# Performance work log

Measured on AMD Instinct MI355X. Metric: run time of the kernel, lower is better.

## Reference

```python
import jax, jax.numpy as jnp
import numpy as np

N_NODES = 100000
N_EDGES = 1600000
IN_FEATS = 128
H1 = 256
H2 = 256
N_CLASSES = 64


def setup_inputs() -> dict:
    key = jax.random.key(0)
    ks = jax.random.split(key, 12)
    x = jax.random.normal(ks[0], (N_NODES, IN_FEATS), dtype=jnp.float32)
    src = jax.random.randint(ks[1], (N_EDGES,), 0, N_NODES, dtype=jnp.int64 if jax.config.jax_enable_x64 else jnp.int32)
    dst = jax.random.randint(ks[2], (N_EDGES,), 0, N_NODES, dtype=jnp.int64 if jax.config.jax_enable_x64 else jnp.int32)
    def lin(kw, kb, fan_in, fan_out):
        bound = 1.0 / np.sqrt(fan_in)
        W = jax.random.uniform(kw, (fan_out, fan_in), minval=-bound, maxval=bound, dtype=jnp.float32)
        b = jax.random.uniform(kb, (fan_out,), minval=-bound, maxval=bound, dtype=jnp.float32)
        return W, b
    W1, b1 = lin(ks[3], ks[4], 2 * IN_FEATS, H1)
    W2, b2 = lin(ks[5], ks[6], 2 * H1, H2)
    W3, b3 = lin(ks[7], ks[8], 2 * H2, N_CLASSES)
    return {"x": x, "src": src, "dst": dst,
            "W1": W1, "b1": b1, "W2": W2, "b2": b2, "W3": W3, "b3": b3}


def _sage_conv(h, src, dst, W, b):
    # message = copy from src node, reduce = mean at dst node (DGL copy_u + mean)
    m = jnp.take(h, src, axis=0)                                  # [E, d]
    s = jax.ops.segment_sum(m, dst, num_segments=N_NODES)         # [N, d]
    deg = jax.ops.segment_sum(jnp.ones((m.shape[0],), h.dtype), dst,
                              num_segments=N_NODES)               # [N]
    h_N = s / jnp.maximum(deg, 1.0)[:, None]                      # isolated nodes -> 0 (DGL behavior)
    h_total = jnp.concatenate([h, h_N], axis=1)                   # [N, 2d]
    return h_total @ W.T + b                                      # dropout inactive at eval (p=0.05)


def reference(x, src, dst, W1, b1, W2, b2, W3, b3):
    h = jax.nn.relu(_sage_conv(x, src, dst, W1, b1))
    h = jax.nn.relu(_sage_conv(h, src, dst, W2, b2))
    return _sage_conv(h, src, dst, W3, b3)
```

## Files before the change

### kernel.cpp

```cpp
#include <hip/hip_runtime.h>
#include <hip/hip_bf16.h>
#include <cstdint>
#include <cstddef>

#define N_NODES 100000
#define N_EDGES 1600000
#define NBUCK   128
#define NPB     782
#define NB_E    ((N_EDGES + 4095) / 4096)

typedef __attribute__((ext_vector_type(8))) short short8;
typedef __attribute__((ext_vector_type(4))) float floatx4;

__device__ inline float bf_lo(unsigned int u) { return __uint_as_float(u << 16); }
__device__ inline float bf_hi(unsigned int u) { return __uint_as_float(u & 0xffff0000u); }
__device__ inline unsigned short f2bf(float f) {
  unsigned int u = __float_as_uint(f);
  u += 0x7fffu + ((u >> 16) & 1u);
  return (unsigned short)(u >> 16);
}

__global__ void cvt_f32_bf16(const float* __restrict__ in,
                             unsigned short* __restrict__ out, int n4) {
  int t = blockIdx.x * blockDim.x + threadIdx.x;
  if (t >= n4) return;
  float4 v = ((const float4*)in)[t];
  ushort4 o;
  o.x = f2bf(v.x); o.y = f2bf(v.y); o.z = f2bf(v.z); o.w = f2bf(v.w);
  ((ushort4*)out)[t] = o;
}

__global__ void cvt_w3cat(const float* __restrict__ W3, unsigned short* __restrict__ out) {
  int t = blockIdx.x * blockDim.x + threadIdx.x;
  if (t >= 128 * 256 / 4) return;
  int idx4 = t * 4;
  int r = idx4 >> 8, c = idx4 & 255;
  float4 v = *(const float4*)(W3 + (size_t)(r & 63) * 512 + (r >> 6) * 256 + c);
  ushort4 o;
  o.x = f2bf(v.x); o.y = f2bf(v.y); o.z = f2bf(v.z); o.w = f2bf(v.w);
  *(ushort4*)(out + (size_t)r * 256 + c) = o;
}

__device__ inline int wave_incl_scan(int v, int lane) {
#pragma unroll
  for (int off = 1; off < 64; off <<= 1) {
    int t = __shfl_up(v, off, 64);
    if (lane >= off) v += t;
  }
  return v;
}

__global__ __launch_bounds__(256)
void pass1a_kernel(const int* __restrict__ dst, int* __restrict__ bucketCount) {
  __shared__ int hist[NBUCK];
  if (threadIdx.x < NBUCK) hist[threadIdx.x] = 0;
  __syncthreads();
#pragma unroll
  for (int i = 0; i < 16; ++i) {
    int e = blockIdx.x * 4096 + i * 256 + threadIdx.x;
    if (e < N_EDGES) atomicAdd(&hist[dst[e] / NPB], 1);
  }
  __syncthreads();
  if (threadIdx.x < NBUCK) atomicAdd(&bucketCount[threadIdx.x], hist[threadIdx.x]);
}

__global__ void scanB_kernel(const int* __restrict__ bucketCount,
                             int* __restrict__ bucketBase, int* __restrict__ gCursorB) {
  __shared__ int wsum[2];
  int t = threadIdx.x, lane = t & 63, wid = t >> 6;
  int v = bucketCount[t];
  int incl = wave_incl_scan(v, lane);
  if (lane == 63) wsum[wid] = incl;
  __syncthreads();
  int off = (wid == 1) ? wsum[0] : 0;
  bucketBase[t] = off + incl - v;
  gCursorB[t]   = off + incl - v;
  if (t == 127) bucketBase[NBUCK] = off + incl;
}

__global__ __launch_bounds__(256)
void pass1b_kernel(const int* __restrict__ src, const int* __restrict__ dst,
                   int* __restrict__ gCursorB, unsigned int* __restrict__ staging) {
  __shared__ int hist[NBUCK];
  if (threadIdx.x < NBUCK) hist[threadIdx.x] = 0;
  __syncthreads();
#pragma unroll
  for (int i = 0; i < 16; ++i) {
    int e = blockIdx.x * 4096 + i * 256 + threadIdx.x;
    if (e < N_EDGES) atomicAdd(&hist[dst[e] / NPB], 1);
  }
  __syncthreads();
  if (threadIdx.x < NBUCK)
    hist[threadIdx.x] = atomicAdd(&gCursorB[threadIdx.x], hist[threadIdx.x]);
  __syncthreads();
#pragma unroll
  for (int i = 0; i < 16; ++i) {
    int e = blockIdx.x * 4096 + i * 256 + threadIdx.x;
    if (e < N_EDGES) {
      int d = dst[e];
      int b = d / NPB;
      int pos = atomicAdd(&hist[b], 1);
      staging[pos] = (unsigned)src[e] | ((unsigned)(d - b * NPB) << 17);
    }
  }
}

__global__ __launch_bounds__(1024)
void pass2_kernel(const unsigned int* __restrict__ staging, const int* __restrict__ bucketBase,
                  int* __restrict__ start, float* __restrict__ invdeg,
                  int* __restrict__ esrc) {
  __shared__ int cnt[1024];
  __shared__ int cur[1024];
  __shared__ int wsum[16];
  const int b = blockIdx.x, tid = threadIdx.x;
  const int lane = tid & 63, wid = tid >> 6;
  const int n0 = b * NPB, n1 = min(n0 + NPB, N_NODES);
  const int nLocal = n1 - n0;
  const int p0 = bucketBase[b], p1 = bucketBase[b + 1];

  cnt[tid] = 0;
  __syncthreads();
  for (int e = p0 + tid; e < p1; e += 1024)
    atomicAdd(&cnt[staging[e] >> 17], 1);
  __syncthreads();

  int c = cnt[tid];
  int incl = wave_incl_scan(c, lane);
  if (lane == 63) wsum[wid] = incl;
  __syncthreads();
  if (wid == 0) {
    int v = (lane < 16) ? wsum[lane] : 0;
    int i2 = wave_incl_scan(v, lane);
    if (lane < 16) wsum[lane] = i2 - v;
  }
  __syncthreads();
  int excl = wsum[wid] + incl - c;
  cur[tid] = excl;
  if (tid < nLocal) {
    start[n0 + tid] = p0 + excl;
    invdeg[n0 + tid] = 1.0f / fmaxf((float)c, 1.0f);
  }
  if (b == NBUCK - 1 && tid == 0) start[N_NODES] = N_EDGES;
  __syncthreads();

  for (int e = p0 + tid; e < p1; e += 1024) {
    unsigned int pr = staging[e];
    int pos = p0 + atomicAdd(&cur[pr >> 17], 1);
    esrc[pos] = (int)(pr & 0x1FFFFu);
  }
}

template<int D>
__global__ __launch_bounds__(256)
void gather_mean(const unsigned short* __restrict__ h,
                 const int* __restrict__ start,
                 const int* __restrict__ esrc,
                 const float* __restrict__ invdeg,
                 unsigned short* __restrict__ hn) {
  int wave = (int)((blockIdx.x * 256 + threadIdx.x) >> 6);
  if (wave >= N_NODES) return;
  int lane = threadIdx.x & 63;
  int s0 = start[wave], s1 = start[wave + 1];
  constexpr int FPL = D / 64;
  float acc[FPL] = {};
  const unsigned short* base = h + lane * FPL;

  int e = s0;
  if constexpr (FPL == 4) {
    for (; e + 4 <= s1; e += 4) {
      int sn0 = esrc[e], sn1 = esrc[e + 1], sn2 = esrc[e + 2], sn3 = esrc[e + 3];
      uint2 p0 = *(const uint2*)(base + (size_t)sn0 * D);
      uint2 p1 = *(const uint2*)(base + (size_t)sn1 * D);
      uint2 p2 = *(const uint2*)(base + (size_t)sn2 * D);
      uint2 p3 = *(const uint2*)(base + (size_t)sn3 * D);
      acc[0] += bf_lo(p0.x) + bf_lo(p1.x) + bf_lo(p2.x) + bf_lo(p3.x);
      acc[1] += bf_hi(p0.x) + bf_hi(p1.x) + bf_hi(p2.x) + bf_hi(p3.x);
      acc[2] += bf_lo(p0.y) + bf_lo(p1.y) + bf_lo(p2.y) + bf_lo(p3.y);
      acc[3] += bf_hi(p0.y) + bf_hi(p1.y) + bf_hi(p2.y) + bf_hi(p3.y);
    }
    for (; e < s1; ++e) {
      int sn = esrc[e];
      uint2 p = *(const uint2*)(base + (size_t)sn * D);
      acc[0] += bf_lo(p.x); acc[1] += bf_hi(p.x);
      acc[2] += bf_lo(p.y); acc[3] += bf_hi(p.y);
    }
  } else {
    for (; e + 4 <= s1; e += 4) {
      int sn0 = esrc[e], sn1 = esrc[e + 1], sn2 = esrc[e + 2], sn3 = esrc[e + 3];
      unsigned int p0 = *(const unsigned int*)(base + (size_t)sn0 * D);
      unsigned int p1 = *(const unsigned int*)(base + (size_t)sn1 * D);
      unsigned int p2 = *(const unsigned int*)(base + (size_t)sn2 * D);
      unsigned int p3 = *(const unsigned int*)(base + (size_t)sn3 * D);
      acc[0] += bf_lo(p0) + bf_lo(p1) + bf_lo(p2) + bf_lo(p3);
      acc[1] += bf_hi(p0) + bf_hi(p1) + bf_hi(p2) + bf_hi(p3);
    }
    for (; e < s1; ++e) {
      int sn = esrc[e];
      unsigned int p = *(const unsigned int*)(base + (size_t)sn * D);
      acc[0] += bf_lo(p); acc[1] += bf_hi(p);
    }
  }

  float inv = invdeg[wave];
  unsigned short* out = hn + (size_t)wave * D + lane * FPL;
  if constexpr (FPL == 4) {
    ushort4 o;
    o.x = f2bf(acc[0] * inv); o.y = f2bf(acc[1] * inv);
    o.z = f2bf(acc[2] * inv); o.w = f2bf(acc[3] * inv);
    *(ushort4*)out = o;
  } else {
    ushort2 o;
    o.x = f2bf(acc[0] * inv); o.y = f2bf(acc[1] * inv);
    *(ushort2*)out = o;
  }
}

__global__ __launch_bounds__(256)
void gather_add64(const unsigned short* __restrict__ Y3,
                  const int* __restrict__ start, const int* __restrict__ esrc,
                  const float* __restrict__ invdeg, float* __restrict__ out) {
  int wave = (int)((blockIdx.x * 256 + threadIdx.x) >> 6);
  if (wave >= N_NODES) return;
  int lane = threadIdx.x & 63;
  int half = lane >> 5, l32 = lane & 31;
  int s0 = start[wave], s1 = start[wave + 1];
  float a0 = 0.f, a1 = 0.f;
  for (int e = s0 + half; e < s1; e += 2) {
    int sn = esrc[e];
    unsigned int p = *(const unsigned int*)(Y3 + (size_t)sn * 64 + 2 * l32);
    a0 += bf_lo(p); a1 += bf_hi(p);
  }
  a0 += __shfl_xor(a0, 32, 64);
  a1 += __shfl_xor(a1, 32, 64);
  if (half == 0) {
    float inv = invdeg[wave];
    float2* q = (float2*)(out + (size_t)wave * 64 + 2 * l32);
    float2 v = *q;
    v.x += inv * a0; v.y += inv * a1;
    *q = v;
  }
}

template<int D, int DOUT, int BN, bool RELU, bool OUTF32, int MODE>
__global__ __launch_bounds__(256)
void sage_gemm(const unsigned short* __restrict__ H,
               const unsigned short* __restrict__ HN,
               const unsigned short* __restrict__ Wb,
               const float* __restrict__ bias,
               void* __restrict__ outp,
               unsigned short* __restrict__ y3) {
  constexpr int K   = (MODE == 1) ? D : 2 * D;
  constexpr int BM  = 128, KC = 32;
  constexpr int NCHUNK = K / KC;
  constexpr int AF  = BM / 16;
  constexpr int BF  = BN / 16;
  constexpr int FR  = AF + BF;
  constexpr int NMF = 4;
  constexpr int NJF = BF / 2;

  __shared__ __align__(16) unsigned short lds0[FR * 512];
  __shared__ __align__(16) unsigned short lds1[FR * 512];

  const int tid  = threadIdx.x;
  const int wave = tid >> 6, lane = tid & 63;
  const int l16  = lane & 15, quad = lane >> 4;
  const int n0   = blockIdx.x * BM;
  const int bn0  = blockIdx.y * BN;
  const int wm   = wave >> 1, wn = wave & 1;

  floatx4 acc[NMF][NJF] = {};

  auto stage = [&](int c, unsigned short* buf) {
    const int kc = c * KC;
    const unsigned short* srcH = (kc < D) ? H : HN;
    const int kb = (kc < D) ? kc : kc - D;
    const int w0 = __builtin_amdgcn_readfirstlane(wave);
#pragma unroll
    for (int i = 0; i < FR / 4; ++i) {
      const int fu = w0 + 4 * i;
      const unsigned short* g;
      if (fu < AF) {
        int row = min(n0 + fu * 16 + l16, N_NODES - 1);
        g = srcH + (size_t)row * D + kb + quad * 8;
      } else {
        int col = bn0 + (fu - AF) * 16 + l16;
        g = Wb + (size_t)col * K + kc + quad * 8;
      }
      __builtin_amdgcn_global_load_lds(
          (const __attribute__((address_space(1))) unsigned int*)g,
          (__attribute__((address_space(3))) unsigned int*)(buf + fu * 512),
          16, 0, 0);
    }
  };

  auto compute = [&](const unsigned short* buf) {
    short8 b[NJF];
#pragma unroll
    for (int jt = 0; jt < NJF; ++jt)
      b[jt] = *(const short8*)(buf + (AF + wn * NJF + jt) * 512 + lane * 8);
#pragma unroll
    for (int mi = 0; mi < NMF; ++mi) {
      short8 a = *(const short8*)(buf + (wm * NMF + mi) * 512 + lane * 8);
#pragma unroll
      for (int jt = 0; jt < NJF; ++jt)
        acc[mi][jt] = __builtin_amdgcn_mfma_f32_16x16x32_bf16(a, b[jt], acc[mi][jt], 0, 0, 0);
    }
  };

  stage(0, lds0);
  __syncthreads();
#pragma unroll 1
  for (int c = 0; c < NCHUNK; c += 2) {
    stage(c + 1, lds1);
    compute(lds0);
    __syncthreads();
    if (c + 2 < NCHUNK) stage(c + 2, lds0);
    compute(lds1);
    __syncthreads();
  }

#pragma unroll
  for (int mi = 0; mi < NMF; ++mi) {
#pragma unroll
    for (int jt = 0; jt < NJF; ++jt) {
      int j = bn0 + wn * (NJF * 16) + jt * 16 + l16;
      float bj = (MODE == 1 && wn == 1) ? 0.0f : bias[j];
#pragma unroll
      for (int r = 0; r < 4; ++r) {
        int node = n0 + wm * 64 + mi * 16 + quad * 4 + r;
        if (node < N_NODES) {
          float v = acc[mi][jt][r];
          if constexpr (MODE == 1) {
            if (wn == 0) ((float*)outp)[(size_t)node * 64 + j] = v + bj;
            else y3[(size_t)node * 64 + (j - 64)] = f2bf(v);
          } else {
            v += bj;
            if (RELU) v = fmaxf(v, 0.0f);
            if (OUTF32) ((float*)outp)[(size_t)node * DOUT + j] = v;
            else ((unsigned short*)outp)[(size_t)node * DOUT + j] = f2bf(v);
          }
        }
      }
    }
  }
}

extern "C" void kernel_launch(void* const* d_in, const int* in_sizes, int n_in,
                              void* d_out, int out_size, void* d_ws, size_t ws_size,
                              hipStream_t stream) {
  const float* x   = (const float*)d_in[0];
  const int*   src = (const int*)d_in[1];
  const int*   dst = (const int*)d_in[2];
  const float* W1 = (const float*)d_in[3];
  const float* b1 = (const float*)d_in[4];
  const float* W2 = (const float*)d_in[5];
  const float* b2 = (const float*)d_in[6];
  const float* W3 = (const float*)d_in[7];
  const float* b3 = (const float*)d_in[8];

  char* ws = (char*)d_ws;
  unsigned short* H0 = (unsigned short*)ws; ws += (size_t)N_NODES * 128 * 2;
  unsigned short* H1 = (unsigned short*)ws; ws += (size_t)N_NODES * 256 * 2;
  unsigned short* H2 = (unsigned short*)ws; ws += (size_t)N_NODES * 256 * 2;
  unsigned short* HN = (unsigned short*)ws; ws += (size_t)N_NODES * 256 * 2;
  unsigned int* staging = (unsigned int*)ws; ws += (size_t)N_EDGES * 4;
  int* esrc   = (int*)ws;  ws += (size_t)N_EDGES * 4;
  int* startp = (int*)ws;  ws += (size_t)(N_NODES + 32) * 4;
  float* invdeg = (float*)ws; ws += (size_t)(N_NODES + 32) * 4;
  int* bucketCount = (int*)ws; ws += 512;
  int* bucketBase  = (int*)ws; ws += 1024;
  int* gCursorB    = (int*)ws; ws += 512;
  unsigned short* Y3 = (unsigned short*)ws; ws += (size_t)N_NODES * 64 * 2;
  unsigned short* Wb1 = (unsigned short*)ws; ws += 256 * 256 * 2;
  unsigned short* Wb2 = (unsigned short*)ws; ws += 256 * 512 * 2;
  unsigned short* Wb3 = (unsigned short*)ws; ws += 128 * 256 * 2;

  hipMemsetAsync(bucketCount, 0, NBUCK * 4, stream);
  pass1a_kernel<<<NB_E, 256, 0, stream>>>(dst, bucketCount);
  scanB_kernel<<<1, 128, 0, stream>>>(bucketCount, bucketBase, gCursorB);
  pass1b_kernel<<<NB_E, 256, 0, stream>>>(src, dst, gCursorB, staging);
  pass2_kernel<<<NBUCK, 1024, 0, stream>>>(staging, bucketBase, startp, invdeg, esrc);

  cvt_f32_bf16<<<(N_NODES * 128 / 4 + 255) / 256, 256, 0, stream>>>(x, H0, N_NODES * 128 / 4);
  cvt_f32_bf16<<<(256 * 256 / 4 + 255) / 256, 256, 0, stream>>>(W1, Wb1, 256 * 256 / 4);
  cvt_f32_bf16<<<(256 * 512 / 4 + 255) / 256, 256, 0, stream>>>(W2, Wb2, 256 * 512 / 4);
  cvt_w3cat<<<(128 * 256 / 4 + 255) / 256, 256, 0, stream>>>(W3, Wb3);

  const int GGRID = (N_NODES * 64 + 255) / 256;
  const int MG = (N_NODES + 127) / 128;

  gather_mean<128><<<GGRID, 256, 0, stream>>>(H0, startp, esrc, invdeg, HN);
  sage_gemm<128, 256, 128, true, false, 0><<<dim3(MG, 2), 256, 0, stream>>>(H0, HN, Wb1, b1, H1, nullptr);

  gather_mean<256><<<GGRID, 256, 0, stream>>>(H1, startp, esrc, invdeg, HN);
  sage_gemm<256, 256, 128, true, false, 0><<<dim3(MG, 2), 256, 0, stream>>>(H1, HN, Wb2, b2, H2, nullptr);

  sage_gemm<256, 128, 128, false, true, 1><<<dim3(MG, 1), 256, 0, stream>>>(H2, nullptr, Wb3, b3, (float*)d_out, Y3);
  gather_add64<<<GGRID, 256, 0, stream>>>(Y3, startp, esrc, invdeg, (float*)d_out);
}
```

Measured before the change: 614.9 us.

## Overlap neighbor gather with GEMM via chunked fused layer kernels

Replaces the separate gather_mean and sage_gemm launches for layers 1 and 2 with a fused kernel that, in each launch, runs GEMM tiles for one node chunk while gathering neighbor means for the next chunk. Nodes are split into four chunks, which gives a software pipeline across five launches per layer. The goal is to hide the memory-bound gather behind the compute-bound GEMM and make better use of the GPU. In exchange it adds launches, mixes LDS-heavy GEMM blocks with lightweight gather blocks (which may hurt occupancy), and uses a hand-written GEMM body whose tiling may differ from the original sage_gemm.

```diff
diff --git a/kernel.cpp b/kernel.cpp
--- a/kernel.cpp
+++ b/kernel.cpp
@@ -151,16 +151,18 @@
 }
 
 template<int D>
-__global__ __launch_bounds__(256)
-void gather_mean(const unsigned short* __restrict__ h,
+__device__ __forceinline__
+void gather_body(int gblk, int node0, int node1,
+                 const unsigned short* __restrict__ h,
                  const int* __restrict__ start,
                  const int* __restrict__ esrc,
                  const float* __restrict__ invdeg,
                  unsigned short* __restrict__ hn) {
-  int wave = (int)((blockIdx.x * 256 + threadIdx.x) >> 6);
-  if (wave >= N_NODES) return;
+  int w = (gblk * 256 + (int)threadIdx.x) >> 6;
+  int node = node0 + w;
+  if (node >= node1) return;
   int lane = threadIdx.x & 63;
-  int s0 = start[wave], s1 = start[wave + 1];
+  int s0 = start[node], s1 = start[node + 1];
   constexpr int FPL = D / 64;
   float acc[FPL] = {};
   const unsigned short* base = h + lane * FPL;
@@ -201,8 +203,8 @@
     }
   }
 
-  float inv = invdeg[wave];
-  unsigned short* out = hn + (size_t)wave * D + lane * FPL;
+  float inv = invdeg[node];
+  unsigned short* out = hn + (size_t)node * D + lane * FPL;
   if constexpr (FPL == 4) {
     ushort4 o;
     o.x = f2bf(acc[0] * inv); o.y = f2bf(acc[1] * inv);
@@ -212,6 +214,119 @@
     ushort2 o;
     o.x = f2bf(acc[0] * inv); o.y = f2bf(acc[1] * inv);
     *(ushort2*)out = o;
+  }
+}
+
+template<int D, bool RELU>
+__device__ __forceinline__
+void gemm_body(int bx, int by,
+               const unsigned short* __restrict__ H,
+               const unsigned short* __restrict__ HN,
+               const unsigned short* __restrict__ Wb,
+               const float* __restrict__ bias,
+               unsigned short* __restrict__ out) {
+  constexpr int K   = 2 * D;
+  constexpr int BM  = 128, KC = 32;
+  constexpr int NCHUNK = K / KC;
+  constexpr int AF  = 8, BF = 8, FR = 16;
+  constexpr int NMF = 4, NJF = 4;
+
+  __shared__ __align__(16) unsigned short lds0[FR * 512];
+  __shared__ __align__(16) unsigned short lds1[FR * 512];
+
+  const int tid  = threadIdx.x;
+  const int wave = tid >> 6, lane = tid & 63;
+  const int l16  = lane & 15, quad = lane >> 4;
+  const int n0   = bx * BM;
+  const int bn0  = by * 128;
+  const int wm   = wave >> 1, wn = wave & 1;
+
+  floatx4 acc[NMF][NJF] = {};
+
+  auto stage = [&](int c, unsigned short* buf) {
+    const int kc = c * KC;
+    const unsigned short* srcH = (kc < D) ? H : HN;
+    const int kb = (kc < D) ? kc : kc - D;
+    const int w0 = __builtin_amdgcn_readfirstlane(wave);
+#pragma unroll
+    for (int i = 0; i < FR / 4; ++i) {
+      const int fu = w0 + 4 * i;
+      const unsigned short* g;
+      if (fu < AF) {
+        int row = min(n0 + fu * 16 + l16, N_NODES - 1);
+        g = srcH + (size_t)row * D + kb + quad * 8;
+      } else {
+        int col = bn0 + (fu - AF) * 16 + l16;
+        g = Wb + (size_t)col * K + kc + quad * 8;
+      }
+      __builtin_amdgcn_global_load_lds(
+          (const __attribute__((address_space(1))) unsigned int*)g,
+          (__attribute__((address_space(3))) unsigned int*)(buf + fu * 512),
+          16, 0, 0);
+    }
+  };
+
+  auto compute = [&](const unsigned short* buf) {
+    short8 b[NJF];
+#pragma unroll
+    for (int jt = 0; jt < NJF; ++jt)
+      b[jt] = *(const short8*)(buf + (AF + wn * NJF + jt) * 512 + lane * 8);
+#pragma unroll
+    for (int mi = 0; mi < NMF; ++mi) {
+      short8 a = *(const short8*)(buf + (wm * NMF + mi) * 512 + lane * 8);
+#pragma unroll
+      for (int jt = 0; jt < NJF; ++jt)
+        acc[mi][jt] = __builtin_amdgcn_mfma_f32_16x16x32_bf16(a, b[jt], acc[mi][jt], 0, 0, 0);
+    }
+  };
+
+  stage(0, lds0);
+  __syncthreads();
+#pragma unroll 1
+  for (int c = 0; c < NCHUNK; c += 2) {
+    stage(c + 1, lds1);
+    compute(lds0);
+    __syncthreads();
+    if (c + 2 < NCHUNK) stage(c + 2, lds0);
+    compute(lds1);
+    __syncthreads();
+  }
+
+#pragma unroll
+  for (int mi = 0; mi < NMF; ++mi) {
+#pragma unroll
+    for (int jt = 0; jt < NJF; ++jt) {
+      int j = bn0 + wn * (NJF * 16) + jt * 16 + l16;
+      float bj = bias[j];
+#pragma unroll
+      for (int r = 0; r < 4; ++r) {
+        int node = n0 + wm * 64 + mi * 16 + quad * 4 + r;
+        if (node < N_NODES) {
+          float v = acc[mi][jt][r] + bj;
+          if (RELU) v = fmaxf(v, 0.0f);
+          out[(size_t)node * 256 + j] = f2bf(v);
+        }
+      }
+    }
+  }
+}
+
+template<int D, bool RELU>
+__global__ __launch_bounds__(256)
+void fused_layer(int tile0, int nGemmBlk, int node0, int node1,
+                 const unsigned short* __restrict__ H,
+                 unsigned short* __restrict__ HN,
+                 const unsigned short* __restrict__ Wb,
+                 const float* __restrict__ bias,
+                 unsigned short* __restrict__ Hout,
+                 const int* __restrict__ start,
+                 const int* __restrict__ esrc,
+                 const float* __restrict__ invdeg) {
+  int b = blockIdx.x;
+  if (b < nGemmBlk) {
+    gemm_body<D, RELU>(tile0 + (b >> 1), b & 1, H, HN, Wb, bias, Hout);
+  } else {
+    gather_body<D>(b - nGemmBlk, node0, node1, H, start, esrc, invdeg, HN);
   }
 }
 
@@ -386,15 +501,39 @@
   cvt_f32_bf16<<<(256 * 512 / 4 + 255) / 256, 256, 0, stream>>>(W2, Wb2, 256 * 512 / 4);
   cvt_w3cat<<<(128 * 256 / 4 + 255) / 256, 256, 0, stream>>>(W3, Wb3);
 
+  static const int tileC[5] = {0, 196, 392, 588, 782};
+  static const int nodeC[5] = {0, 25088, 50176, 75264, N_NODES};
+
+  {
+    int gb0 = (nodeC[1] - nodeC[0] + 3) / 4;
+    fused_layer<128, true><<<gb0, 256, 0, stream>>>(
+        0, 0, nodeC[0], nodeC[1], H0, HN, Wb1, b1, H1, startp, esrc, invdeg);
+    for (int c = 0; c < 4; ++c) {
+      int nG = (tileC[c + 1] - tileC[c]) * 2;
+      int n0g = (c < 3) ? nodeC[c + 1] : 0;
+      int n1g = (c < 3) ? nodeC[c + 2] : 0;
+      int ng  = (c < 3) ? (n1g - n0g + 3) / 4 : 0;
+      fused_layer<128, true><<<nG + ng, 256, 0, stream>>>(
+          tileC[c], nG, n0g, n1g, H0, HN, Wb1, b1, H1, startp, esrc, invdeg);
+    }
+  }
+
+  {
+    int gb0 = (nodeC[1] - nodeC[0] + 3) / 4;
+    fused_layer<256, true><<<gb0, 256, 0, stream>>>(
+        0, 0, nodeC[0], nodeC[1], H1, HN, Wb2, b2, H2, startp, esrc, invdeg);
+    for (int c = 0; c < 4; ++c) {
+      int nG = (tileC[c + 1] - tileC[c]) * 2;
+      int n0g = (c < 3) ? nodeC[c + 1] : 0;
+      int n1g = (c < 3) ? nodeC[c + 2] : 0;
+      int ng  = (c < 3) ? (n1g - n0g + 3) / 4 : 0;
+      fused_layer<256, true><<<nG + ng, 256, 0, stream>>>(
+          tileC[c], nG, n0g, n1g, H1, HN, Wb2, b2, H2, startp, esrc, invdeg);
+    }
+  }
+
+  const int MG = (N_NODES + 127) / 128;
   const int GGRID = (N_NODES * 64 + 255) / 256;
-  const int MG = (N_NODES + 127) / 128;
-
-  gather_mean<128><<<GGRID, 256, 0, stream>>>(H0, startp, esrc, invdeg, HN);
-  sage_gemm<128, 256, 128, true, false, 0><<<dim3(MG, 2), 256, 0, stream>>>(H0, HN, Wb1, b1, H1, nullptr);
-
-  gather_mean<256><<<GGRID, 256, 0, stream>>>(H1, startp, esrc, invdeg, HN);
-  sage_gemm<256, 256, 128, true, false, 0><<<dim3(MG, 2), 256, 0, stream>>>(H1, HN, Wb2, b2, H2, nullptr);
-
   sage_gemm<256, 128, 128, false, true, 1><<<dim3(MG, 1), 256, 0, stream>>>(H2, nullptr, Wb3, b3, (float*)d_out, Y3);
   gather_add64<<<GGRID, 256, 0, stream>>>(Y3, startp, esrc, invdeg, (float*)d_out);
 }
```

Result: slower. 778.5 us (+26.6%).

## Fuse preprocessing launches and use per-block histograms; unroll final gather loads

Applied to the files above, without the earlier changes.

Merges the dst histogram pass and all four fp32-to-bf16 conversions into a single front kernel. Each edge block now writes its own bucket histogram, so the scan kernel can compute per-block offsets. That removes the memset, the global atomics and the duplicate histogram pass in pass1b. It also makes the bucket scatter order deterministic. Separately, the final 64-wide gather now issues 8 independent loads per iteration into two accumulator pairs to raise memory-level parallelism. The cost is a serial loop over about 391 blocks in the single-block scan kernel.

```diff
diff --git a/kernel.cpp b/kernel.cpp
--- a/kernel.cpp
+++ b/kernel.cpp
@@ -8,6 +8,12 @@
 #define NBUCK   128
 #define NPB     782
 #define NB_E    ((N_EDGES + 4095) / 4096)
+
+#define FK_X    NB_E
+#define FK_W1   (FK_X + 12500)
+#define FK_W2   (FK_W1 + 64)
+#define FK_W3   (FK_W2 + 128)
+#define FK_END  (FK_W3 + 32)
 
 typedef __attribute__((ext_vector_type(8))) short short8;
 typedef __attribute__((ext_vector_type(4))) float floatx4;
@@ -20,25 +26,47 @@
   return (unsigned short)(u >> 16);
 }
 
-__global__ void cvt_f32_bf16(const float* __restrict__ in,
-                             unsigned short* __restrict__ out, int n4) {
-  int t = blockIdx.x * blockDim.x + threadIdx.x;
-  if (t >= n4) return;
+__device__ inline void cvt4_body(const float* __restrict__ in,
+                                 unsigned short* __restrict__ out, int t) {
   float4 v = ((const float4*)in)[t];
   ushort4 o;
   o.x = f2bf(v.x); o.y = f2bf(v.y); o.z = f2bf(v.z); o.w = f2bf(v.w);
   ((ushort4*)out)[t] = o;
 }
 
-__global__ void cvt_w3cat(const float* __restrict__ W3, unsigned short* __restrict__ out) {
-  int t = blockIdx.x * blockDim.x + threadIdx.x;
-  if (t >= 128 * 256 / 4) return;
-  int idx4 = t * 4;
-  int r = idx4 >> 8, c = idx4 & 255;
-  float4 v = *(const float4*)(W3 + (size_t)(r & 63) * 512 + (r >> 6) * 256 + c);
-  ushort4 o;
-  o.x = f2bf(v.x); o.y = f2bf(v.y); o.z = f2bf(v.z); o.w = f2bf(v.w);
-  *(ushort4*)(out + (size_t)r * 256 + c) = o;
+__global__ __launch_bounds__(256)
+void front_kernel(const int* __restrict__ dst, int* __restrict__ blockHist,
+                  const float* __restrict__ x,  unsigned short* __restrict__ H0,
+                  const float* __restrict__ W1, unsigned short* __restrict__ Wb1,
+                  const float* __restrict__ W2, unsigned short* __restrict__ Wb2,
+                  const float* __restrict__ W3, unsigned short* __restrict__ Wb3) {
+  __shared__ int hist[NBUCK];
+  const int b = blockIdx.x, tid = threadIdx.x;
+  if (b < FK_X) {
+    if (tid < NBUCK) hist[tid] = 0;
+    __syncthreads();
+#pragma unroll
+    for (int i = 0; i < 16; ++i) {
+      int e = b * 4096 + i * 256 + tid;
+      if (e < N_EDGES) atomicAdd(&hist[dst[e] / NPB], 1);
+    }
+    __syncthreads();
+    if (tid < NBUCK) blockHist[b * NBUCK + tid] = hist[tid];
+  } else if (b < FK_W1) {
+    cvt4_body(x, H0, (b - FK_X) * 256 + tid);
+  } else if (b < FK_W2) {
+    cvt4_body(W1, Wb1, (b - FK_W1) * 256 + tid);
+  } else if (b < FK_W3) {
+    cvt4_body(W2, Wb2, (b - FK_W2) * 256 + tid);
+  } else {
+    int t = (b - FK_W3) * 256 + tid;
+    int idx4 = t * 4;
+    int r = idx4 >> 8, c = idx4 & 255;
+    float4 v = *(const float4*)(W3 + (size_t)(r & 63) * 512 + (r >> 6) * 256 + c);
+    ushort4 o;
+    o.x = f2bf(v.x); o.y = f2bf(v.y); o.z = f2bf(v.z); o.w = f2bf(v.w);
+    *(ushort4*)(Wb3 + (size_t)r * 256 + c) = o;
+  }
 }
 
 __device__ inline int wave_incl_scan(int v, int lane) {
@@ -50,48 +78,33 @@
   return v;
 }
 
-__global__ __launch_bounds__(256)
-void pass1a_kernel(const int* __restrict__ dst, int* __restrict__ bucketCount) {
-  __shared__ int hist[NBUCK];
-  if (threadIdx.x < NBUCK) hist[threadIdx.x] = 0;
-  __syncthreads();
-#pragma unroll
-  for (int i = 0; i < 16; ++i) {
-    int e = blockIdx.x * 4096 + i * 256 + threadIdx.x;
-    if (e < N_EDGES) atomicAdd(&hist[dst[e] / NPB], 1);
-  }
-  __syncthreads();
-  if (threadIdx.x < NBUCK) atomicAdd(&bucketCount[threadIdx.x], hist[threadIdx.x]);
-}
-
-__global__ void scanB_kernel(const int* __restrict__ bucketCount,
-                             int* __restrict__ bucketBase, int* __restrict__ gCursorB) {
+__global__ void scanB_kernel(const int* __restrict__ blockHist,
+                             int* __restrict__ bucketBase, int* __restrict__ blockOfs) {
   __shared__ int wsum[2];
   int t = threadIdx.x, lane = t & 63, wid = t >> 6;
-  int v = bucketCount[t];
-  int incl = wave_incl_scan(v, lane);
+  int total = 0;
+#pragma unroll 4
+  for (int blk = 0; blk < NB_E; ++blk) total += blockHist[blk * NBUCK + t];
+  int incl = wave_incl_scan(total, lane);
   if (lane == 63) wsum[wid] = incl;
   __syncthreads();
   int off = (wid == 1) ? wsum[0] : 0;
-  bucketBase[t] = off + incl - v;
-  gCursorB[t]   = off + incl - v;
+  int base = off + incl - total;
+  bucketBase[t] = base;
   if (t == 127) bucketBase[NBUCK] = off + incl;
+  int running = base;
+#pragma unroll 4
+  for (int blk = 0; blk < NB_E; ++blk) {
+    blockOfs[blk * NBUCK + t] = running;
+    running += blockHist[blk * NBUCK + t];
+  }
 }
 
 __global__ __launch_bounds__(256)
 void pass1b_kernel(const int* __restrict__ src, const int* __restrict__ dst,
-                   int* __restrict__ gCursorB, unsigned int* __restrict__ staging) {
+                   const int* __restrict__ blockOfs, unsigned int* __restrict__ staging) {
   __shared__ int hist[NBUCK];
-  if (threadIdx.x < NBUCK) hist[threadIdx.x] = 0;
-  __syncthreads();
-#pragma unroll
-  for (int i = 0; i < 16; ++i) {
-    int e = blockIdx.x * 4096 + i * 256 + threadIdx.x;
-    if (e < N_EDGES) atomicAdd(&hist[dst[e] / NPB], 1);
-  }
-  __syncthreads();
-  if (threadIdx.x < NBUCK)
-    hist[threadIdx.x] = atomicAdd(&gCursorB[threadIdx.x], hist[threadIdx.x]);
+  if (threadIdx.x < NBUCK) hist[threadIdx.x] = blockOfs[blockIdx.x * NBUCK + threadIdx.x];
   __syncthreads();
 #pragma unroll
   for (int i = 0; i < 16; ++i) {
@@ -224,12 +237,22 @@
   int lane = threadIdx.x & 63;
   int half = lane >> 5, l32 = lane & 31;
   int s0 = start[wave], s1 = start[wave + 1];
-  float a0 = 0.f, a1 = 0.f;
-  for (int e = s0 + half; e < s1; e += 2) {
-    int sn = esrc[e];
-    unsigned int p = *(const unsigned int*)(Y3 + (size_t)sn * 64 + 2 * l32);
-    a0 += bf_lo(p); a1 += bf_hi(p);
-  }
+  const unsigned short* ybase = Y3 + 2 * l32;
+  float a0 = 0.f, a1 = 0.f, b0 = 0.f, b1 = 0.f;
+  for (int base = s0 + half; base < s1; base += 16) {
+    unsigned int p[8];
+#pragma unroll
+    for (int k = 0; k < 8; ++k) {
+      int e = base + 2 * k;
+      p[k] = (e < s1) ? *(const unsigned int*)(ybase + (size_t)esrc[e] * 64) : 0u;
+    }
+#pragma unroll
+    for (int k = 0; k < 8; k += 2) {
+      a0 += bf_lo(p[k]);     a1 += bf_hi(p[k]);
+      b0 += bf_lo(p[k + 1]); b1 += bf_hi(p[k + 1]);
+    }
+  }
+  a0 += b0; a1 += b1;
   a0 += __shfl_xor(a0, 32, 64);
   a1 += __shfl_xor(a1, 32, 64);
   if (half == 0) {
@@ -367,24 +390,18 @@
   int* esrc   = (int*)ws;  ws += (size_t)N_EDGES * 4;
   int* startp = (int*)ws;  ws += (size_t)(N_NODES + 32) * 4;
   float* invdeg = (float*)ws; ws += (size_t)(N_NODES + 32) * 4;
-  int* bucketCount = (int*)ws; ws += 512;
   int* bucketBase  = (int*)ws; ws += 1024;
-  int* gCursorB    = (int*)ws; ws += 512;
+  int* blockHist   = (int*)ws; ws += (size_t)NB_E * NBUCK * 4;
+  int* blockOfs    = (int*)ws; ws += (size_t)NB_E * NBUCK * 4;
   unsigned short* Y3 = (unsigned short*)ws; ws += (size_t)N_NODES * 64 * 2;
   unsigned short* Wb1 = (unsigned short*)ws; ws += 256 * 256 * 2;
   unsigned short* Wb2 = (unsigned short*)ws; ws += 256 * 512 * 2;
   unsigned short* Wb3 = (unsigned short*)ws; ws += 128 * 256 * 2;
 
-  hipMemsetAsync(bucketCount, 0, NBUCK * 4, stream);
-  pass1a_kernel<<<NB_E, 256, 0, stream>>>(dst, bucketCount);
-  scanB_kernel<<<1, 128, 0, stream>>>(bucketCount, bucketBase, gCursorB);
-  pass1b_kernel<<<NB_E, 256, 0, stream>>>(src, dst, gCursorB, staging);
+  front_kernel<<<FK_END, 256, 0, stream>>>(dst, blockHist, x, H0, W1, Wb1, W2, Wb2, W3, Wb3);
+  scanB_kernel<<<1, 128, 0, stream>>>(blockHist, bucketBase, blockOfs);
+  pass1b_kernel<<<NB_E, 256, 0, stream>>>(src, dst, blockOfs, staging);
   pass2_kernel<<<NBUCK, 1024, 0, stream>>>(staging, bucketBase, startp, invdeg, esrc);
-
-  cvt_f32_bf16<<<(N_NODES * 128 / 4 + 255) / 256, 256, 0, stream>>>(x, H0, N_NODES * 128 / 4);
-  cvt_f32_bf16<<<(256 * 256 / 4 + 255) / 256, 256, 0, stream>>>(W1, Wb1, 256 * 256 / 4);
-  cvt_f32_bf16<<<(256 * 512 / 4 + 255) / 256, 256, 0, stream>>>(W2, Wb2, 256 * 512 / 4);
-  cvt_w3cat<<<(128 * 256 / 4 + 255) / 256, 256, 0, stream>>>(W3, Wb3);
 
   const int GGRID = (N_NODES * 64 + 255) / 256;
   const int MG = (N_NODES + 127) / 128;
```

Result: no change. 613.8 us (-0.2%).
